# Optimization experiments

Hardware: AMD Instinct MI355X
Metric: run time of the kernel (lower is better)

Reference implementation:

```python
import jax, jax.numpy as jnp
from jax import lax
import numpy as np

N, E, L, H, B, R = 12800, 204800, 24, 128, 64, 8
VN, VA = 100, 20


def _p(key, *shape):
    return jax.random.normal(key, shape, dtype=jnp.float32) * 0.05


def setup_inputs() -> dict:
    key = jax.random.key(0)
    ks = jax.random.split(key, 32)
    inp = {
        'nodeTypes': jax.random.randint(ks[0], (N,), 0, VN),
        'edge_index': jax.random.randint(ks[1], (2, E), 0, N),
        'edge_attr': jax.random.randint(ks[2], (E,), 0, R),
        'bs': jnp.repeat(jnp.arange(B, dtype=jnp.int32), N // B),
        'sequence_input': jax.random.uniform(ks[3], (N, L), dtype=jnp.float32),
        'nodes_bs': jnp.full((B,), N // B, dtype=jnp.int32),
        'len_seq': jnp.full((B,), L, dtype=jnp.int32),
        'action_input': jax.random.randint(ks[4], (B,), 0, VA),
        # parameters (RGCN weights SHARED across the 2 layers, as in the source)
        'emb_nodes_w': _p(ks[5], VN, H),
        'emb_actions_w': _p(ks[6], VA, H),
        'rgcn_W': _p(ks[7], R, H, H),
        'rgcn_root': _p(ks[8], H, H),
        'rgcn_b': _p(ks[9], H),
        'gru_Wih': _p(ks[10], 3 * H, H),
        'gru_Whh': _p(ks[11], 3 * H, H),
        'gru_bih': _p(ks[12], 3 * H),
        'gru_bhh': _p(ks[13], 3 * H),
        'linA_w': _p(ks[14], H, H),
        'linA_b': _p(ks[15], H),
        'linAf_w': _p(ks[16], VA, H),
        'linAf_b': _p(ks[17], VA),
        'linN_w': _p(ks[18], H, 2 * H),
        'linN_b': _p(ks[19], H),
        'linNf_w': _p(ks[20], 1, H),
        'linNf_b': _p(ks[21], 1),
        'fin_w': _p(ks[22], H, H),
        'fin_b': _p(ks[23], H),
        'finf_w': _p(ks[24], 1, H),
        'finf_b': _p(ks[25], 1),
    }
    return inp


def _rgcn(x, src, dst, etype, W, Wroot, b):
    # PyG RGCNConv: per-relation mean aggregation, then per-relation weight, plus root + bias
    comb = dst * R + etype  # combined (node, relation) segment id
    msg = jax.ops.segment_sum(x[src], comb, num_segments=N * R)  # [N*R, H]
    cnt = jax.ops.segment_sum(jnp.ones((src.shape[0],), x.dtype), comb, num_segments=N * R)
    mean = (msg / jnp.maximum(cnt, 1.0)[:, None]).reshape(N, R, H)
    return jnp.einsum('nrh,rhd->nd', mean, W) + x @ Wroot + b


def _gru(x_seq, h0, Wih, Whh, bih, bhh):
    # torch GRU gate order: r, z, n ; x_seq [B, T, H]
    def step(h, x):
        gi = x @ Wih.T + bih
        gh = h @ Whh.T + bhh
        i_r, i_z, i_n = jnp.split(gi, 3, axis=-1)
        h_r, h_z, h_n = jnp.split(gh, 3, axis=-1)
        r = jax.nn.sigmoid(i_r + h_r)
        z = jax.nn.sigmoid(i_z + h_z)
        n = jnp.tanh(i_n + r * h_n)
        h_new = (1.0 - z) * n + z * h
        return h_new, h_new
    _, ys = lax.scan(step, h0, jnp.swapaxes(x_seq, 0, 1))
    return jnp.swapaxes(ys, 0, 1)


def _seg_softmax(x, seg, nseg):
    m = jax.ops.segment_max(x, seg, num_segments=nseg)
    e = jnp.exp(x - m[seg])
    s = jax.ops.segment_sum(e, seg, num_segments=nseg)
    return e / s[seg]


def reference(nodeTypes, edge_index, edge_attr, bs, sequence_input, nodes_bs, len_seq,
              action_input, emb_nodes_w, emb_actions_w, rgcn_W, rgcn_root, rgcn_b,
              gru_Wih, gru_Whh, gru_bih, gru_bhh, linA_w, linA_b, linAf_w, linAf_b,
              linN_w, linN_b, linNf_w, linNf_b, fin_w, fin_b, finf_w, finf_b):
    src, dst = edge_index[0], edge_index[1]
    x = emb_nodes_w[nodeTypes]
    for _ in range(2):  # shared-weight RGCN layers + ReLU
        x = jax.nn.relu(_rgcn(x, src, dst, edge_attr, rgcn_W, rgcn_root, rgcn_b))
    nodeEmb = x  # [N, H]

    cnt = jax.ops.segment_sum(jnp.ones((N,), x.dtype), bs, num_segments=B)
    h_G = jax.ops.segment_sum(nodeEmb, bs, num_segments=B) / cnt[:, None]  # [B, H]

    action = jax.nn.relu(h_G @ linA_w.T + linA_b) @ linAf_w.T + linAf_b  # [B, VA]
    final = jax.nn.sigmoid(jax.nn.relu(h_G @ fin_w.T + fin_b) @ finf_w.T + finf_b)  # [B, 1]

    sos = emb_actions_w[action_input][:, None, :]  # [B, 1, H]
    # scatter-sum of per-timestep weighted node embeddings -> [B, L, H]
    emb_seq = sequence_input[:, :, None] * nodeEmb[:, None, :]  # [N, L, H]
    agg = jax.ops.segment_sum(emb_seq, bs, num_segments=B)
    input_gru = jnp.concatenate([sos, agg], axis=1)[:, :L]  # len_seq == L drops last step
    seq = _gru(input_gru, h_G, gru_Wih, gru_Whh, gru_bih, gru_bhh)  # [B, L, H]

    # linNodes(cat(out_gru, nodeEmb)) computed without materializing the [N,L,2H] concat
    part1 = jnp.einsum('blh,oh->blo', seq, linN_w[:, :H])[bs]      # [N, L, H]
    part2 = nodeEmb @ linN_w[:, H:].T                               # [N, H]
    hidden = jax.nn.relu(part1 + part2[:, None, :] + linN_b)       # [N, L, H]
    logits = jnp.einsum('nlh,h->nl', hidden, linNf_w[0]) + linNf_b[0]  # [N, L]
    nodes_final = _seg_softmax(logits, bs, B)
    return (action, nodes_final, final)
```

## Files before the change

### kernel.cpp

```cpp
#include <hip/hip_runtime.h>
#include <math.h>

#define NN 12800
#define NE 204800
#define LL 24
#define HH 128
#define BB 64
#define RR 8
#define VAx 20
#define KC 1152
#define CHK 8
#define PS 16

typedef __attribute__((ext_vector_type(8))) short bf16x8;
typedef __attribute__((ext_vector_type(4))) float f32x4;

__device__ inline unsigned short f2bf(float f) {
  unsigned u = __float_as_uint(f);
  unsigned r = u + 0x7FFF + ((u >> 16) & 1);
  return (unsigned short)(r >> 16);
}
__device__ inline float bf2f(unsigned short s) {
  return __uint_as_float(((unsigned)s) << 16);
}
__device__ inline unsigned packbf(float lo, float hi) {
  return (unsigned)f2bf(lo) | ((unsigned)f2bf(hi) << 16);
}

__global__ void k_prep(const float* __restrict__ rgcnW, const float* __restrict__ rgcnRoot,
                       unsigned short* __restrict__ wcatT,
                       const float* __restrict__ linN_w, unsigned short* __restrict__ linN2bt,
                       const float* __restrict__ Wih, unsigned short* __restrict__ Wihbt,
                       const float* __restrict__ Whh, float* __restrict__ WhhT,
                       const float* __restrict__ linA_w, float* __restrict__ linAT,
                       const float* __restrict__ fin_w, float* __restrict__ finT,
                       unsigned short* __restrict__ linN1bt,
                       const int* __restrict__ nt, const float* __restrict__ embN,
                       unsigned int* __restrict__ x, int* __restrict__ deg) {
  int idx = blockIdx.x * 256 + threadIdx.x;
  if (idx < HH * KC) {
    int d = idx / KC, k = idx - d * KC;
    float v = (k < 1024) ? rgcnW[(k >> 7) * (HH * HH) + (k & 127) * HH + d]
                         : rgcnRoot[(k - 1024) * HH + d];
    wcatT[idx] = f2bf(v);
    return;
  }
  idx -= HH * KC;
  if (idx < HH * HH) {
    int d = idx >> 7, k = idx & 127;
    linN2bt[idx] = f2bf(linN_w[d * 2 * HH + HH + k]);
    return;
  }
  idx -= HH * HH;
  if (idx < 3 * HH * HH) {
    Wihbt[idx] = f2bf(Wih[idx]);
    return;
  }
  idx -= 3 * HH * HH;
  if (idx < 3 * HH * HH) {
    int r = idx / HH, c = idx - r * HH;
    WhhT[c * 384 + r] = Whh[r * HH + c];
    return;
  }
  idx -= 3 * HH * HH;
  if (idx < HH * HH) {
    int r = idx >> 7, c = idx & 127;
    linAT[c * HH + r] = linA_w[r * HH + c];
    return;
  }
  idx -= HH * HH;
  if (idx < HH * HH) {
    int r = idx >> 7, c = idx & 127;
    finT[c * HH + r] = fin_w[r * HH + c];
    return;
  }
  idx -= HH * HH;
  if (idx < HH * HH) {
    int o = idx >> 7, k = idx & 127;
    linN1bt[idx] = f2bf(linN_w[o * 2 * HH + k]);
    return;
  }
  idx -= HH * HH;
  if (idx < NN * 64) {
    int n = idx >> 6, p = idx & 63;
    const float* e = embN + (size_t)nt[n] * HH + p * 2;
    x[idx] = packbf(e[0], e[1]);
    return;
  }
  idx -= NN * 64;
  if (idx < NN * PS) deg[idx] = 0;
}
#define PREP_TOTAL (HH * KC + HH * HH + 3 * HH * HH + 3 * HH * HH + HH * HH + HH * HH + HH * HH + NN * 64 + NN * PS)

__global__ void k_count(const int* __restrict__ edst, int* __restrict__ deg,
                        const int* __restrict__ bs, int* __restrict__ bptr) {
  int i = blockIdx.x * 256 + threadIdx.x;
  if (i < NE) atomicAdd(&deg[edst[i] * PS], 1);
  if (i < NN) {
    int b = bs[i];
    if (i == 0 || bs[i - 1] != b) bptr[b] = i;
    if (i == NN - 1) bptr[BB] = NN;
  }
}

__global__ __launch_bounds__(1024) void k_scane(const int* __restrict__ deg,
                                                int* __restrict__ indptr,
                                                int* __restrict__ cur) {
  __shared__ int ws[16];
  int tid = threadIdx.x;
  const int per = (NN + 1023) >> 10;
  int i0 = tid * per;
  int s = 0;
  for (int k = 0; k < per; ++k) {
    int i = i0 + k;
    if (i < NN) s += deg[i * PS];
  }
  int lane = tid & 63, wv = tid >> 6;
  int incl = s;
#pragma unroll
  for (int off = 1; off < 64; off <<= 1) {
    int t = __shfl_up(incl, off);
    if (lane >= off) incl += t;
  }
  if (lane == 63) ws[wv] = incl;
  __syncthreads();
  if (tid < 16) {
    int v = ws[tid];
    int inc = v;
#pragma unroll
    for (int off = 1; off < 16; off <<= 1) {
      int t = __shfl_up(inc, off);
      if (tid >= off) inc += t;
    }
    ws[tid] = inc - v;
  }
  __syncthreads();
  int run = ws[wv] + incl - s;
  for (int k = 0; k < per; ++k) {
    int i = i0 + k;
    if (i < NN) {
      indptr[i] = run;
      cur[i * PS] = run;
      run += deg[i * PS];
      if (i == NN - 1) indptr[NN] = run;
    }
  }
}

__global__ void k_scattere(const int* __restrict__ esrc, const int* __restrict__ edst,
                           const int* __restrict__ erel, int* __restrict__ cur,
                           int* __restrict__ esort) {
  int i = blockIdx.x * 256 + threadIdx.x;
  if (i >= NE) return;
  int p = atomicAdd(&cur[edst[i] * PS], 1);
  esort[p] = esrc[i] | (erel[i] << 16);
}

__global__ __launch_bounds__(256) void k_agg(const unsigned int* __restrict__ x,
                                             const int* __restrict__ indptr,
                                             const int* __restrict__ esort,
                                             unsigned int* __restrict__ A, int n0, int nc) {
  int wid = ((blockIdx.x * 256) + threadIdx.x) >> 6;
  int lane = threadIdx.x & 63;
  if (wid >= nc) return;
  int n = n0 + wid;
  float a0=0,a1=0,a2=0,a3=0,a4=0,a5=0,a6=0,a7=0;
  float b0=0,b1=0,b2=0,b3=0,b4=0,b5=0,b6=0,b7=0;
  int c0=0,c1=0,c2=0,c3=0,c4=0,c5=0,c6=0,c7=0;
  int e0 = indptr[n], e1 = indptr[n + 1];

#define ACCV(RV, VV)                                                              \
  {                                                                               \
    float v0_ = bf2f((unsigned short)((VV) & 0xFFFF));                            \
    float v1_ = bf2f((unsigned short)((VV) >> 16));                               \
    switch (RV) {                                                                 \
      case 0: a0 += v0_; b0 += v1_; c0++; break;                                  \
      case 1: a1 += v0_; b1 += v1_; c1++; break;                                  \
      case 2: a2 += v0_; b2 += v1_; c2++; break;                                  \
      case 3: a3 += v0_; b3 += v1_; c3++; break;                                  \
      case 4: a4 += v0_; b4 += v1_; c4++; break;                                  \
      case 5: a5 += v0_; b5 += v1_; c5++; break;                                  \
      case 6: a6 += v0_; b6 += v1_; c6++; break;                                  \
      default: a7 += v0_; b7 += v1_; c7++; break;                                 \
    }                                                                             \
  }

  int e = e0;
  for (; e + 8 <= e1; e += 8) {
    int pk0 = esort[e + 0], pk1 = esort[e + 1], pk2 = esort[e + 2], pk3 = esort[e + 3];
    int pk4 = esort[e + 4], pk5 = esort[e + 5], pk6 = esort[e + 6], pk7 = esort[e + 7];
    unsigned v0 = x[(size_t)(pk0 & 0xFFFF) * 64 + lane];
    unsigned v1 = x[(size_t)(pk1 & 0xFFFF) * 64 + lane];
    unsigned v2 = x[(size_t)(pk2 & 0xFFFF) * 64 + lane];
    unsigned v3 = x[(size_t)(pk3 & 0xFFFF) * 64 + lane];
    unsigned v4 = x[(size_t)(pk4 & 0xFFFF) * 64 + lane];
    unsigned v5 = x[(size_t)(pk5 & 0xFFFF) * 64 + lane];
    unsigned v6 = x[(size_t)(pk6 & 0xFFFF) * 64 + lane];
    unsigned v7 = x[(size_t)(pk7 & 0xFFFF) * 64 + lane];
    ACCV(pk0 >> 16, v0);
    ACCV(pk1 >> 16, v1);
    ACCV(pk2 >> 16, v2);
    ACCV(pk3 >> 16, v3);
    ACCV(pk4 >> 16, v4);
    ACCV(pk5 >> 16, v5);
    ACCV(pk6 >> 16, v6);
    ACCV(pk7 >> 16, v7);
  }
  for (; e + 4 <= e1; e += 4) {
    int pk0 = esort[e + 0], pk1 = esort[e + 1], pk2 = esort[e + 2], pk3 = esort[e + 3];
    unsigned v0 = x[(size_t)(pk0 & 0xFFFF) * 64 + lane];
    unsigned v1 = x[(size_t)(pk1 & 0xFFFF) * 64 + lane];
    unsigned v2 = x[(size_t)(pk2 & 0xFFFF) * 64 + lane];
    unsigned v3 = x[(size_t)(pk3 & 0xFFFF) * 64 + lane];
    ACCV(pk0 >> 16, v0);
    ACCV(pk1 >> 16, v1);
    ACCV(pk2 >> 16, v2);
    ACCV(pk3 >> 16, v3);
  }
  for (; e < e1; ++e) {
    int pk = esort[e];
    unsigned v = x[(size_t)(pk & 0xFFFF) * 64 + lane];
    ACCV(pk >> 16, v);
  }
#undef ACCV

  unsigned int* Ar = A + (size_t)wid * (KC / 2);
  float i0 = 1.0f / (float)(c0 > 0 ? c0 : 1);
  float i1 = 1.0f / (float)(c1 > 0 ? c1 : 1);
  float i2 = 1.0f / (float)(c2 > 0 ? c2 : 1);
  float i3 = 1.0f / (float)(c3 > 0 ? c3 : 1);
  float i4 = 1.0f / (float)(c4 > 0 ? c4 : 1);
  float i5 = 1.0f / (float)(c5 > 0 ? c5 : 1);
  float i6 = 1.0f / (float)(c6 > 0 ? c6 : 1);
  float i7 = 1.0f / (float)(c7 > 0 ? c7 : 1);
  Ar[0 * 64 + lane] = packbf(a0 * i0, b0 * i0);
  Ar[1 * 64 + lane] = packbf(a1 * i1, b1 * i1);
  Ar[2 * 64 + lane] = packbf(a2 * i2, b2 * i2);
  Ar[3 * 64 + lane] = packbf(a3 * i3, b3 * i3);
  Ar[4 * 64 + lane] = packbf(a4 * i4, b4 * i4);
  Ar[5 * 64 + lane] = packbf(a5 * i5, b5 * i5);
  Ar[6 * 64 + lane] = packbf(a6 * i6, b6 * i6);
  Ar[7 * 64 + lane] = packbf(a7 * i7, b7 * i7);
  Ar[512 + lane] = x[n * 64 + lane];
}

__global__ __launch_bounds__(256) void k_mgemm_rg32(const unsigned short* __restrict__ Abf,
                                                    const unsigned short* __restrict__ BTbf,
                                                    const float* __restrict__ bias,
                                                    unsigned short* __restrict__ C) {
  __shared__ unsigned int ldsu[(4096 + 16384) / 4];
  char* ldsc = (char*)ldsu;
  int tid = threadIdx.x;
  int m0 = blockIdx.x * 32;
  int w = tid >> 6, l = tid & 63;
  int lrow = l & 15, lg = l >> 4;
  int rowg = w & 1, colg = w >> 1;
  f32x4 acc[4] = {};

  const char* Ab = (const char*)Abf;
  const char* Bb = (const char*)BTbf;
  for (int kt = 0; kt < KC / 64; ++kt) {
    int k0 = kt << 6;
    {
      int slot = tid;
      int row = slot >> 3;
      int colb = (slot & 7) << 4;
      size_t srcb = ((size_t)(m0 + row) * KC + k0) * 2 + (size_t)(colb ^ ((row & 7) << 4));
      __builtin_amdgcn_global_load_lds((const unsigned int*)(Ab + srcb),
                                       (unsigned int*)(ldsc + slot * 16), 16, 0, 0);
    }
#pragma unroll
    for (int i = 0; i < 4; ++i) {
      int slot = i * 256 + tid;
      int row = slot >> 3;
      int colb = (slot & 7) << 4;
      size_t srcb = ((size_t)row * KC + k0) * 2 + (size_t)(colb ^ ((row & 7) << 4));
      __builtin_amdgcn_global_load_lds((const unsigned int*)(Bb + srcb),
                                       (unsigned int*)(ldsc + 4096 + slot * 16), 16, 0, 0);
    }
    __syncthreads();
#pragma unroll
    for (int h = 0; h < 2; ++h) {
      int arow = rowg * 16 + lrow;
      bf16x8 af = *(const bf16x8*)(ldsc + arow * 128 +
                                   ((h * 64 + lg * 16) ^ ((arow & 7) << 4)));
#pragma unroll
      for (int c = 0; c < 4; ++c) {
        int brow = (colg * 4 + c) * 16 + lrow;
        bf16x8 bfr = *(const bf16x8*)(ldsc + 4096 + brow * 128 +
                                      ((h * 64 + lg * 16) ^ ((brow & 7) << 4)));
        acc[c] = __builtin_amdgcn_mfma_f32_16x16x32_bf16(af, bfr, acc[c], 0, 0, 0);
      }
    }
    __syncthreads();
  }
#pragma unroll
  for (int c = 0; c < 4; ++c) {
    int gn = (colg * 4 + c) * 16 + lrow;
    float bv = bias[gn];
#pragma unroll
    for (int r = 0; r < 4; ++r) {
      int gm = m0 + rowg * 16 + lg * 4 + r;
      float v = fmaxf(acc[c][r] + bv, 0.f);
      C[(size_t)gm * HH + gn] = f2bf(v);
    }
  }
}

template <int OUTMODE>
__global__ __launch_bounds__(256) void k_mgemm(const unsigned short* __restrict__ Abf, int lda,
                                               const unsigned short* __restrict__ BTbf, int ldb,
                                               const float* __restrict__ bias,
                                               void* __restrict__ C, int ldc, int M, int K) {
  __shared__ unsigned int ldsu[(8192 + 16384) / 4];
  char* ldsc = (char*)ldsu;
  int tid = threadIdx.x;
  int m0 = blockIdx.x * 64;
  int n0c = blockIdx.y * 128;
  int w = tid >> 6, l = tid & 63;
  int lrow = l & 15, lg = l >> 4;
  f32x4 acc[8] = {};

  const char* Ab = (const char*)Abf;
  const char* Bb = (const char*)(BTbf + (size_t)n0c * ldb);
  int KT = K >> 6;
  for (int kt = 0; kt < KT; ++kt) {
    int k0 = kt << 6;
#pragma unroll
    for (int i = 0; i < 2; ++i) {
      int slot = i * 256 + tid;
      int row = slot >> 3;
      int colb = (slot & 7) << 4;
      int gr = m0 + row;
      gr = gr < M ? gr : M - 1;
      size_t srcb = ((size_t)gr * lda + k0) * 2 + (size_t)(colb ^ ((row & 7) << 4));
      __builtin_amdgcn_global_load_lds((const unsigned int*)(Ab + srcb),
                                       (unsigned int*)(ldsc + slot * 16), 16, 0, 0);
    }
#pragma unroll
    for (int i = 0; i < 4; ++i) {
      int slot = i * 256 + tid;
      int row = slot >> 3;
      int colb = (slot & 7) << 4;
      size_t srcb = ((size_t)row * ldb + k0) * 2 + (size_t)(colb ^ ((row & 7) << 4));
      __builtin_amdgcn_global_load_lds((const unsigned int*)(Bb + srcb),
                                       (unsigned int*)(ldsc + 8192 + slot * 16), 16, 0, 0);
    }
    __syncthreads();
#pragma unroll
    for (int h = 0; h < 2; ++h) {
      int arow = w * 16 + lrow;
      bf16x8 af = *(const bf16x8*)(ldsc + arow * 128 +
                                   ((h * 64 + lg * 16) ^ ((arow & 7) << 4)));
#pragma unroll
      for (int c = 0; c < 8; ++c) {
        int brow = c * 16 + lrow;
        bf16x8 bf = *(const bf16x8*)(ldsc + 8192 + brow * 128 +
                                     ((h * 64 + lg * 16) ^ ((brow & 7) << 4)));
        acc[c] = __builtin_amdgcn_mfma_f32_16x16x32_bf16(af, bf, acc[c], 0, 0, 0);
      }
    }
    __syncthreads();
  }
#pragma unroll
  for (int c = 0; c < 8; ++c) {
#pragma unroll
    for (int r = 0; r < 4; ++r) {
      int gm = m0 + w * 16 + lg * 4 + r;
      if (gm >= M) continue;
      int gn = n0c + c * 16 + lrow;
      float v = acc[c][r];
      if (OUTMODE == 1) {
        v = fmaxf(v + bias[gn], 0.f);
        ((unsigned short*)C)[(size_t)gm * ldc + gn] = f2bf(v);
      } else if (OUTMODE == 2) {
        ((float*)C)[(size_t)gm * ldc + gn] = v + bias[gn];
      } else {
        ((float*)C)[(size_t)gm * ldc + gn] = v;
      }
    }
  }
}

__global__ __launch_bounds__(256) void k_mgemm_gp(const unsigned short* __restrict__ ig,
                                                  const unsigned short* __restrict__ Wihbt,
                                                  const float* __restrict__ bih,
                                                  float* __restrict__ gi,
                                                  const unsigned short* __restrict__ nodeEmb,
                                                  const unsigned short* __restrict__ linN2bt,
                                                  float* __restrict__ part2) {
  __shared__ unsigned int ldsu[(8192 + 16384) / 4];
  char* ldsc = (char*)ldsu;
  int tid = threadIdx.x;
  int bid = blockIdx.x;
  const unsigned short* Abf;
  const unsigned short* BTbf;
  const float* bias;
  float* Cf;
  int m0, ldc, withbias;
  const int GIB = (BB * LL / 64) * 3;
  if (bid < GIB) {
    int mb = bid / 3, nc = bid % 3;
    Abf = ig;
    BTbf = Wihbt + (size_t)(nc * 128) * HH;
    bias = bih + nc * 128;
    Cf = gi + nc * 128;
    m0 = mb * 64;
    ldc = 3 * HH;
    withbias = 1;
  } else {
    Abf = nodeEmb;
    BTbf = linN2bt;
    bias = nullptr;
    Cf = part2;
    m0 = (bid - GIB) * 64;
    ldc = HH;
    withbias = 0;
  }
  int w = tid >> 6, l = tid & 63;
  int lrow = l & 15, lg = l >> 4;
  f32x4 acc[8] = {};
  const char* Ab = (const char*)Abf;
  const char* Bb = (const char*)BTbf;
  for (int kt = 0; kt < 2; ++kt) {
    int k0 = kt << 6;
#pragma unroll
    for (int i = 0; i < 2; ++i) {
      int slot = i * 256 + tid;
      int row = slot >> 3;
      int colb = (slot & 7) << 4;
      size_t srcb = ((size_t)(m0 + row) * HH + k0) * 2 + (size_t)(colb ^ ((row & 7) << 4));
      __builtin_amdgcn_global_load_lds((const unsigned int*)(Ab + srcb),
                                       (unsigned int*)(ldsc + slot * 16), 16, 0, 0);
    }
#pragma unroll
    for (int i = 0; i < 4; ++i) {
      int slot = i * 256 + tid;
      int row = slot >> 3;
      int colb = (slot & 7) << 4;
      size_t srcb = ((size_t)row * HH + k0) * 2 + (size_t)(colb ^ ((row & 7) << 4));
      __builtin_amdgcn_global_load_lds((const unsigned int*)(Bb + srcb),
                                       (unsigned int*)(ldsc + 8192 + slot * 16), 16, 0, 0);
    }
    __syncthreads();
#pragma unroll
    for (int h = 0; h < 2; ++h) {
      int arow = w * 16 + lrow;
      bf16x8 af = *(const bf16x8*)(ldsc + arow * 128 +
                                   ((h * 64 + lg * 16) ^ ((arow & 7) << 4)));
#pragma unroll
      for (int c = 0; c < 8; ++c) {
        int brow = c * 16 + lrow;
        bf16x8 bfr = *(const bf16x8*)(ldsc + 8192 + brow * 128 +
                                      ((h * 64 + lg * 16) ^ ((brow & 7) << 4)));
        acc[c] = __builtin_amdgcn_mfma_f32_16x16x32_bf16(af, bfr, acc[c], 0, 0, 0);
      }
    }
    __syncthreads();
  }
#pragma unroll
  for (int c = 0; c < 8; ++c) {
    int gn = c * 16 + lrow;
    float bv = withbias ? bias[gn] : 0.f;
#pragma unroll
    for (int r = 0; r < 4; ++r) {
      int gm = m0 + w * 16 + lg * 4 + r;
      Cf[(size_t)gm * ldc + gn] = acc[c][r] + bv;
    }
  }
}

__global__ __launch_bounds__(256) void k_aggS_part(const float* __restrict__ seqin,
                                                   const unsigned short* __restrict__ x,
                                                   const int* __restrict__ bptr,
                                                   float* __restrict__ part) {
  int bc = blockIdx.x, b = bc >> 3, c = bc & 7;
  int h = threadIdx.x & 127, l0 = threadIdx.x >> 7;
  int i0 = bptr[b], i1 = bptr[b + 1];
  int len = i1 - i0;
  int per = (len + CHK - 1) / CHK;
  int j0 = i0 + c * per;
  int j1 = j0 + per;
  if (j1 > i1) j1 = i1;
  float acc[12] = {};
  float esum = 0.f;
  for (int n = j0; n < j1; ++n) {
    float e = bf2f(x[n * HH + h]);
    esum += e;
    const float* srow = seqin + (size_t)n * LL;
#pragma unroll
    for (int t = 0; t < 12; ++t) acc[t] = fmaf(srow[l0 + 2 * t], e, acc[t]);
  }
  float* p = part + (size_t)bc * 25 * HH + h;
#pragma unroll
  for (int t = 0; t < 12; ++t) p[(l0 + 2 * t) * HH] = acc[t];
  if (l0 == 0) p[24 * HH] = esum;
}

__global__ void k_aggS_red(const float* __restrict__ part, const int* __restrict__ bptr,
                           const float* __restrict__ embA, const int* __restrict__ act,
                           unsigned short* __restrict__ ig, float* __restrict__ hG) {
  int idx = blockIdx.x * 256 + threadIdx.x;
  if (idx >= BB * 25 * HH) return;
  int h = idx & 127;
  int rem = idx >> 7;
  int l = rem % 25, b = rem / 25;
  if (l == 23) {
    ig[((size_t)b * LL) * HH + h] = f2bf(embA[(size_t)act[b] * HH + h]);
    return;
  }
  float s = 0.f;
#pragma unroll
  for (int c = 0; c < CHK; ++c) s += part[(((size_t)(b * CHK + c)) * 25 + l) * HH + h];
  if (l == 24) {
    int len = bptr[b + 1] - bptr[b];
    hG[b * HH + h] = s / (float)len;
  } else {
    ig[((size_t)b * LL + l + 1) * HH + h] = f2bf(s);
  }
}

__global__ __launch_bounds__(128) void k_heads(const float* __restrict__ hG,
                                               const float* __restrict__ linAT,
                                               const float* __restrict__ linA_b,
                                               const float* __restrict__ linAf_w,
                                               const float* __restrict__ linAf_b,
                                               const float* __restrict__ finT,
                                               const float* __restrict__ fin_b,
                                               const float* __restrict__ finf_w,
                                               const float* __restrict__ finf_b,
                                               float* __restrict__ outA,
                                               float* __restrict__ outF) {
  int b = blockIdx.x >> 1, which = blockIdx.x & 1, j = threadIdx.x;
  __shared__ float hsh[HH], t1[HH];
  hsh[j] = hG[b * HH + j];
  __syncthreads();
  const float* Wt = which ? finT : linAT;
  const float* bb = which ? fin_b : linA_b;
  float s = bb[j];
  for (int k = 0; k < HH; ++k) s = fmaf(hsh[k], Wt[k * HH + j], s);
  t1[j] = fmaxf(s, 0.f);
  __syncthreads();
  if (which == 0) {
    if (j < VAx) {
      float o = linAf_b[j];
      for (int k = 0; k < HH; ++k) o = fmaf(t1[k], linAf_w[j * HH + k], o);
      outA[b * VAx + j] = o;
    }
  } else if (j == 0) {
    float o = finf_b[0];
    for (int k = 0; k < HH; ++k) o = fmaf(t1[k], finf_w[k], o);
    outF[b] = 1.f / (1.f + expf(-o));
  }
}

__global__ __launch_bounds__(384) void k_gru(const float* __restrict__ gi,
                                             const float* __restrict__ WhhT,
                                             const float* __restrict__ bhh,
                                             const float* __restrict__ hG,
                                             unsigned short* __restrict__ seqout) {
  int b = blockIdx.x, tid = threadIdx.x;
  int gate = tid >> 7, j = tid & 127;
  __shared__ float h[HH];
  __shared__ float sz[HH], sg[HH];
  float w[HH];
#pragma unroll
  for (int k = 0; k < HH; ++k) w[k] = WhhT[k * 384 + tid];
  float bh = bhh[tid];
  if (tid < HH) h[tid] = hG[b * HH + tid];
  __syncthreads();
  const float* gib = gi + (size_t)b * LL * 384;
  for (int t = 0; t < LL; ++t) {
    float giv = gib[t * 384 + tid];
    float gin = (gate == 0) ? gib[t * 384 + 256 + j] : 0.f;
    float hj = h[j];
    float g0 = 0.f, g1 = 0.f, g2 = 0.f, g3 = 0.f;
    const float4* h4 = (const float4*)h;
#pragma unroll
    for (int k4 = 0; k4 < HH / 4; ++k4) {
      float4 hv = h4[k4];
      g0 = fmaf(w[4 * k4 + 0], hv.x, g0);
      g1 = fmaf(w[4 * k4 + 1], hv.y, g1);
      g2 = fmaf(w[4 * k4 + 2], hv.z, g2);
      g3 = fmaf(w[4 * k4 + 3], hv.w, g3);
    }
    float g = bh + ((g0 + g1) + (g2 + g3));
    float r = 0.f;
    if (gate == 0) {
      r = 1.f / (1.f + expf(-(giv + g)));
    } else if (gate == 1) {
      sz[j] = 1.f / (1.f + expf(-(giv + g)));
    } else {
      sg[j] = g;
    }
    __syncthreads();
    if (gate == 0) {
      float n = tanhf(gin + r * sg[j]);
      float z = sz[j];
      float hn = (1.f - z) * n + z * hj;
      h[j] = hn;
      seqout[((size_t)b * LL + t) * HH + j] = f2bf(hn);
    }
    __syncthreads();
  }
}

__global__ __launch_bounds__(256) void k_logits(const float* __restrict__ part1,
                                                const float* __restrict__ part2,
                                                const float* __restrict__ linN_b,
                                                const float* __restrict__ linNf_w,
                                                const float* __restrict__ linNf_b,
                                                const int* __restrict__ bs,
                                                float* __restrict__ logits) {
  int wid = ((blockIdx.x * 256) + threadIdx.x) >> 6;
  int lane = threadIdx.x & 63;
  if (wid >= NN) return;
  int n = wid;
  int b = bs[n];
  float p2a = part2[n * HH + lane] + linN_b[lane];
  float p2b = part2[n * HH + 64 + lane] + linN_b[64 + lane];
  float wa = linNf_w[lane], wb = linNf_w[64 + lane];
  const float* p1 = part1 + (size_t)b * LL * HH;
  float bf = linNf_b[0];
  for (int l = 0; l < LL; ++l) {
    float v = fmaxf(p1[l * HH + lane] + p2a, 0.f) * wa +
              fmaxf(p1[l * HH + 64 + lane] + p2b, 0.f) * wb;
#pragma unroll
    for (int off = 32; off > 0; off >>= 1) v += __shfl_down(v, off);
    if (lane == 0) logits[n * LL + l] = v + bf;
  }
}

__global__ __launch_bounds__(64) void k_softmax(const float* __restrict__ logits,
                                                const int* __restrict__ bptr,
                                                float* __restrict__ outN) {
  int b = blockIdx.x / LL, l = blockIdx.x % LL;
  int lane = threadIdx.x;
  int i0 = bptr[b], i1 = bptr[b + 1];
  float m = -1e30f;
  for (int i = i0 + lane; i < i1; i += 64) m = fmaxf(m, logits[i * LL + l]);
#pragma unroll
  for (int off = 32; off > 0; off >>= 1) m = fmaxf(m, __shfl_xor(m, off));
  float s = 0.f;
  for (int i = i0 + lane; i < i1; i += 64) s += expf(logits[i * LL + l] - m);
#pragma unroll
  for (int off = 32; off > 0; off >>= 1) s += __shfl_xor(s, off);
  float inv = 1.f / s;
  for (int i = i0 + lane; i < i1; i += 64) {
    outN[i * LL + l] = expf(logits[i * LL + l] - m) * inv;
  }
}

extern "C" void kernel_launch(void* const* d_in, const int* in_sizes, int n_in,
                              void* d_out, int out_size, void* d_ws, size_t ws_size,
                              hipStream_t stream) {
  const int* nodeTypes = (const int*)d_in[0];
  const int* esrc = (const int*)d_in[1];
  const int* edst = esrc + NE;
  const int* erel = (const int*)d_in[2];
  const int* bs = (const int*)d_in[3];
  const float* seqin = (const float*)d_in[4];
  const int* actin = (const int*)d_in[7];
  const float* embN = (const float*)d_in[8];
  const float* embA = (const float*)d_in[9];
  const float* rgcnW = (const float*)d_in[10];
  const float* rgcnRoot = (const float*)d_in[11];
  const float* rgcnB = (const float*)d_in[12];
  const float* Wih = (const float*)d_in[13];
  const float* Whh = (const float*)d_in[14];
  const float* bih = (const float*)d_in[15];
  const float* bhh = (const float*)d_in[16];
  const float* linA_w = (const float*)d_in[17];
  const float* linA_b = (const float*)d_in[18];
  const float* linAf_w = (const float*)d_in[19];
  const float* linAf_b = (const float*)d_in[20];
  const float* linN_w = (const float*)d_in[21];
  const float* linN_b = (const float*)d_in[22];
  const float* linNf_w = (const float*)d_in[23];
  const float* linNf_b = (const float*)d_in[24];
  const float* fin_w = (const float*)d_in[25];
  const float* fin_b = (const float*)d_in[26];
  const float* finf_w = (const float*)d_in[27];
  const float* finf_b = (const float*)d_in[28];

  float* outA = (float*)d_out;
  float* outNodes = outA + BB * VAx;
  float* outF = outNodes + (size_t)NN * LL;

  char* basep = (char*)d_ws;
  size_t off = 0;
  auto alloc = [&](size_t bytes) -> void* {
    void* p = basep + off;
    off = (off + bytes + 255) & ~(size_t)255;
    return p;
  };

  unsigned int* x = (unsigned int*)alloc(sizeof(unsigned int) * NN * 64);
  unsigned int* x2 = (unsigned int*)alloc(sizeof(unsigned int) * NN * 64);
  float* hG = (float*)alloc(sizeof(float) * BB * HH);
  unsigned short* wcatT = (unsigned short*)alloc(sizeof(unsigned short) * HH * KC);
  unsigned short* linN2bt = (unsigned short*)alloc(sizeof(unsigned short) * HH * HH);
  unsigned short* Wihbt = (unsigned short*)alloc(sizeof(unsigned short) * 3 * HH * HH);
  unsigned short* linN1bt = (unsigned short*)alloc(sizeof(unsigned short) * HH * HH);
  float* WhhT = (float*)alloc(sizeof(float) * HH * 3 * HH);
  float* linAT = (float*)alloc(sizeof(float) * HH * HH);
  float* finT = (float*)alloc(sizeof(float) * HH * HH);
  float* part = (float*)alloc(sizeof(float) * BB * CHK * 25 * HH);
  unsigned short* ig = (unsigned short*)alloc(sizeof(unsigned short) * BB * LL * HH);
  float* gi = (float*)alloc(sizeof(float) * BB * LL * 3 * HH);
  unsigned short* seqb = (unsigned short*)alloc(sizeof(unsigned short) * BB * LL * HH);
  float* part1 = (float*)alloc(sizeof(float) * BB * LL * HH);
  float* part2 = (float*)alloc(sizeof(float) * NN * HH);
  float* logitsB = (float*)alloc(sizeof(float) * NN * LL);
  int* deg = (int*)alloc(sizeof(int) * NN * PS);
  int* cur = (int*)alloc(sizeof(int) * NN * PS);
  int* indptr = (int*)alloc(sizeof(int) * (NN + 1));
  int* esort = (int*)alloc(sizeof(int) * NE);
  int* bptr = (int*)alloc(sizeof(int) * (BB + 1));

  size_t remain = (ws_size > off) ? (ws_size - off) : 0;
  int NCk = NN;
  while ((size_t)NCk * KC * 2 > remain && NCk > 100) NCk >>= 1;
  unsigned int* A = (unsigned int*)alloc((size_t)NCk * (KC / 2) * sizeof(unsigned int));

  k_prep<<<(PREP_TOTAL + 255) / 256, 256, 0, stream>>>(
      rgcnW, rgcnRoot, wcatT, linN_w, linN2bt, Wih, Wihbt, Whh, WhhT, linA_w, linAT,
      fin_w, finT, linN1bt, nodeTypes, embN, x, deg);

  k_count<<<(NE + 255) / 256, 256, 0, stream>>>(edst, deg, bs, bptr);
  k_scane<<<1, 1024, 0, stream>>>(deg, indptr, cur);
  k_scattere<<<(NE + 255) / 256, 256, 0, stream>>>(esrc, edst, erel, cur, esort);

  const unsigned int* xin = x;
  unsigned int* xout = x2;
  for (int layer = 0; layer < 2; ++layer) {
    for (int n0 = 0; n0 < NN; n0 += NCk) {
      int nc = NN - n0 < NCk ? NN - n0 : NCk;
      k_agg<<<(nc + 3) / 4, 256, 0, stream>>>(xin, indptr, esort, A, n0, nc);
      k_mgemm_rg32<<<nc / 32, 256, 0, stream>>>(
          (const unsigned short*)A, wcatT, rgcnB,
          (unsigned short*)xout + (size_t)n0 * HH);
    }
    const unsigned int* t = xin;
    xin = xout;
    xout = (unsigned int*)t;
  }
  const unsigned short* nodeEmb = (const unsigned short*)xin;

  k_aggS_part<<<BB * CHK, 256, 0, stream>>>(seqin, nodeEmb, bptr, part);
  k_aggS_red<<<(BB * 25 * HH + 255) / 256, 256, 0, stream>>>(part, bptr, embA, actin, ig, hG);

  k_mgemm_gp<<<(BB * LL / 64) * 3 + NN / 64, 256, 0, stream>>>(ig, Wihbt, bih, gi,
                                                               nodeEmb, linN2bt, part2);

  k_heads<<<2 * BB, HH, 0, stream>>>(hG, linAT, linA_b, linAf_w, linAf_b, finT, fin_b,
                                     finf_w, finf_b, outA, outF);

  k_gru<<<BB, 384, 0, stream>>>(gi, WhhT, bhh, hG, seqb);

  {
    dim3 g((BB * LL) / 64, 1);
    k_mgemm<0><<<g, 256, 0, stream>>>(seqb, HH, linN1bt, HH, nullptr, (void*)part1, HH,
                                      BB * LL, HH);
  }
  k_logits<<<NN / 4, 256, 0, stream>>>(part1, part2, linN_b, linNf_w, linNf_b, bs, logitsB);
  k_softmax<<<BB * LL, 64, 0, stream>>>(logitsB, bptr, outNodes);
}
```

Measured before the change: 248.5 us.

## Fuse edge counting into prep, heads into GEMM, logits with softmax

Folds the degree counting and batch pointer computation into the prep kernel, using a memset to zero degrees. The small MLP heads run as extra blocks of the GEMM kernel. The logits and segment softmax become a single per-(graph,timestep) kernel that keeps logits in shared memory, removing the intermediate logits buffer and several launches. The fused softmax kernel re-reads part2 for every timestep and assumes at most 256 nodes per graph.

```diff
diff --git a/kernel.cpp b/kernel.cpp
--- a/kernel.cpp
+++ b/kernel.cpp
@@ -36,7 +36,9 @@
                        const float* __restrict__ fin_w, float* __restrict__ finT,
                        unsigned short* __restrict__ linN1bt,
                        const int* __restrict__ nt, const float* __restrict__ embN,
-                       unsigned int* __restrict__ x, int* __restrict__ deg) {
+                       unsigned int* __restrict__ x, int* __restrict__ deg,
+                       const int* __restrict__ edst, const int* __restrict__ bs,
+                       int* __restrict__ bptr) {
   int idx = blockIdx.x * 256 + threadIdx.x;
   if (idx < HH * KC) {
     int d = idx / KC, k = idx - d * KC;
@@ -88,20 +90,18 @@
     return;
   }
   idx -= NN * 64;
-  if (idx < NN * PS) deg[idx] = 0;
-}
-#define PREP_TOTAL (HH * KC + HH * HH + 3 * HH * HH + 3 * HH * HH + HH * HH + HH * HH + HH * HH + NN * 64 + NN * PS)
-
-__global__ void k_count(const int* __restrict__ edst, int* __restrict__ deg,
-                        const int* __restrict__ bs, int* __restrict__ bptr) {
-  int i = blockIdx.x * 256 + threadIdx.x;
-  if (i < NE) atomicAdd(&deg[edst[i] * PS], 1);
-  if (i < NN) {
-    int b = bs[i];
-    if (i == 0 || bs[i - 1] != b) bptr[b] = i;
-    if (i == NN - 1) bptr[BB] = NN;
-  }
-}
+  if (idx < NE) {
+    atomicAdd(&deg[edst[idx] * PS], 1);
+    return;
+  }
+  idx -= NE;
+  if (idx < NN) {
+    int b = bs[idx];
+    if (idx == 0 || bs[idx - 1] != b) bptr[b] = idx;
+    if (idx == NN - 1) bptr[BB] = NN;
+  }
+}
+#define PREP_TOTAL (HH * KC + HH * HH + 3 * HH * HH + 3 * HH * HH + HH * HH + HH * HH + HH * HH + NN * 64 + NE + NN)
 
 __global__ __launch_bounds__(1024) void k_scane(const int* __restrict__ deg,
                                                 int* __restrict__ indptr,
@@ -382,23 +382,62 @@
   }
 }
 
-__global__ __launch_bounds__(256) void k_mgemm_gp(const unsigned short* __restrict__ ig,
+__global__ __launch_bounds__(256) void k_gp_heads(const unsigned short* __restrict__ ig,
                                                   const unsigned short* __restrict__ Wihbt,
                                                   const float* __restrict__ bih,
                                                   float* __restrict__ gi,
                                                   const unsigned short* __restrict__ nodeEmb,
                                                   const unsigned short* __restrict__ linN2bt,
-                                                  float* __restrict__ part2) {
+                                                  float* __restrict__ part2,
+                                                  const float* __restrict__ hG,
+                                                  const float* __restrict__ linAT,
+                                                  const float* __restrict__ linA_b,
+                                                  const float* __restrict__ linAf_w,
+                                                  const float* __restrict__ linAf_b,
+                                                  const float* __restrict__ finT,
+                                                  const float* __restrict__ fin_b,
+                                                  const float* __restrict__ finf_w,
+                                                  const float* __restrict__ finf_b,
+                                                  float* __restrict__ outA,
+                                                  float* __restrict__ outF) {
+  int tid = threadIdx.x;
+  int bid = blockIdx.x;
+  const int GIB = (BB * LL / 64) * 3;
+  const int GEMMB = GIB + NN / 64;
+  if (bid >= GEMMB) {
+    int hb = bid - GEMMB;
+    int b = hb >> 1, which = hb & 1, j = tid;
+    __shared__ float hsh[HH], t1[HH];
+    if (j < HH) hsh[j] = hG[b * HH + j];
+    __syncthreads();
+    if (j < HH) {
+      const float* Wt = which ? finT : linAT;
+      const float* bb = which ? fin_b : linA_b;
+      float s = bb[j];
+      for (int k = 0; k < HH; ++k) s = fmaf(hsh[k], Wt[k * HH + j], s);
+      t1[j] = fmaxf(s, 0.f);
+    }
+    __syncthreads();
+    if (which == 0) {
+      if (j < VAx) {
+        float o = linAf_b[j];
+        for (int k = 0; k < HH; ++k) o = fmaf(t1[k], linAf_w[j * HH + k], o);
+        outA[b * VAx + j] = o;
+      }
+    } else if (j == 0) {
+      float o = finf_b[0];
+      for (int k = 0; k < HH; ++k) o = fmaf(t1[k], finf_w[k], o);
+      outF[b] = 1.f / (1.f + expf(-o));
+    }
+    return;
+  }
   __shared__ unsigned int ldsu[(8192 + 16384) / 4];
   char* ldsc = (char*)ldsu;
-  int tid = threadIdx.x;
-  int bid = blockIdx.x;
   const unsigned short* Abf;
   const unsigned short* BTbf;
   const float* bias;
   float* Cf;
   int m0, ldc, withbias;
-  const int GIB = (BB * LL / 64) * 3;
   if (bid < GIB) {
     int mb = bid / 3, nc = bid % 3;
     Abf = ig;
@@ -520,40 +559,6 @@
   }
 }
 
-__global__ __launch_bounds__(128) void k_heads(const float* __restrict__ hG,
-                                               const float* __restrict__ linAT,
-                                               const float* __restrict__ linA_b,
-                                               const float* __restrict__ linAf_w,
-                                               const float* __restrict__ linAf_b,
-                                               const float* __restrict__ finT,
-                                               const float* __restrict__ fin_b,
-                                               const float* __restrict__ finf_w,
-                                               const float* __restrict__ finf_b,
-                                               float* __restrict__ outA,
-                                               float* __restrict__ outF) {
-  int b = blockIdx.x >> 1, which = blockIdx.x & 1, j = threadIdx.x;
-  __shared__ float hsh[HH], t1[HH];
-  hsh[j] = hG[b * HH + j];
-  __syncthreads();
-  const float* Wt = which ? finT : linAT;
-  const float* bb = which ? fin_b : linA_b;
-  float s = bb[j];
-  for (int k = 0; k < HH; ++k) s = fmaf(hsh[k], Wt[k * HH + j], s);
-  t1[j] = fmaxf(s, 0.f);
-  __syncthreads();
-  if (which == 0) {
-    if (j < VAx) {
-      float o = linAf_b[j];
-      for (int k = 0; k < HH; ++k) o = fmaf(t1[k], linAf_w[j * HH + k], o);
-      outA[b * VAx + j] = o;
-    }
-  } else if (j == 0) {
-    float o = finf_b[0];
-    for (int k = 0; k < HH; ++k) o = fmaf(t1[k], finf_w[k], o);
-    outF[b] = 1.f / (1.f + expf(-o));
-  }
-}
-
 __global__ __launch_bounds__(384) void k_gru(const float* __restrict__ gi,
                                              const float* __restrict__ WhhT,
                                              const float* __restrict__ bhh,
@@ -605,50 +610,49 @@
   }
 }
 
-__global__ __launch_bounds__(256) void k_logits(const float* __restrict__ part1,
-                                                const float* __restrict__ part2,
-                                                const float* __restrict__ linN_b,
-                                                const float* __restrict__ linNf_w,
-                                                const float* __restrict__ linNf_b,
-                                                const int* __restrict__ bs,
-                                                float* __restrict__ logits) {
-  int wid = ((blockIdx.x * 256) + threadIdx.x) >> 6;
-  int lane = threadIdx.x & 63;
-  if (wid >= NN) return;
-  int n = wid;
-  int b = bs[n];
-  float p2a = part2[n * HH + lane] + linN_b[lane];
-  float p2b = part2[n * HH + 64 + lane] + linN_b[64 + lane];
-  float wa = linNf_w[lane], wb = linNf_w[64 + lane];
-  const float* p1 = part1 + (size_t)b * LL * HH;
+__global__ __launch_bounds__(256) void k_logsm(const float* __restrict__ part1,
+                                               const float* __restrict__ part2,
+                                               const float* __restrict__ linN_b,
+                                               const float* __restrict__ linNf_w,
+                                               const float* __restrict__ linNf_b,
+                                               const int* __restrict__ bptr,
+                                               float* __restrict__ outN) {
+  int bl = blockIdx.x;
+  int b = bl / LL, l = bl % LL;
+  __shared__ float p1b[HH], wsh[HH], lg[256], red[8];
+  int tid = threadIdx.x;
+  int w = tid >> 6, lane = tid & 63;
+  if (tid < HH) {
+    p1b[tid] = part1[((size_t)b * LL + l) * HH + tid] + linN_b[tid];
+    wsh[tid] = linNf_w[tid];
+  }
+  __syncthreads();
+  int i0 = bptr[b], i1 = bptr[b + 1];
+  int len = i1 - i0;
   float bf = linNf_b[0];
-  for (int l = 0; l < LL; ++l) {
-    float v = fmaxf(p1[l * HH + lane] + p2a, 0.f) * wa +
-              fmaxf(p1[l * HH + 64 + lane] + p2b, 0.f) * wb;
+  for (int i = i0 + w; i < i1; i += 4) {
+    const float* p2 = part2 + (size_t)i * HH;
+    float v = fmaxf(p1b[lane] + p2[lane], 0.f) * wsh[lane] +
+              fmaxf(p1b[64 + lane] + p2[64 + lane], 0.f) * wsh[64 + lane];
 #pragma unroll
     for (int off = 32; off > 0; off >>= 1) v += __shfl_down(v, off);
-    if (lane == 0) logits[n * LL + l] = v + bf;
-  }
-}
-
-__global__ __launch_bounds__(64) void k_softmax(const float* __restrict__ logits,
-                                                const int* __restrict__ bptr,
-                                                float* __restrict__ outN) {
-  int b = blockIdx.x / LL, l = blockIdx.x % LL;
-  int lane = threadIdx.x;
-  int i0 = bptr[b], i1 = bptr[b + 1];
-  float m = -1e30f;
-  for (int i = i0 + lane; i < i1; i += 64) m = fmaxf(m, logits[i * LL + l]);
+    if (lane == 0) lg[i - i0] = v + bf;
+  }
+  __syncthreads();
+  float m = (tid < len) ? lg[tid] : -1e30f;
 #pragma unroll
   for (int off = 32; off > 0; off >>= 1) m = fmaxf(m, __shfl_xor(m, off));
-  float s = 0.f;
-  for (int i = i0 + lane; i < i1; i += 64) s += expf(logits[i * LL + l] - m);
+  if (lane == 0) red[w] = m;
+  __syncthreads();
+  m = fmaxf(fmaxf(red[0], red[1]), fmaxf(red[2], red[3]));
+  float e = (tid < len) ? expf(lg[tid] - m) : 0.f;
+  float s = e;
 #pragma unroll
   for (int off = 32; off > 0; off >>= 1) s += __shfl_xor(s, off);
-  float inv = 1.f / s;
-  for (int i = i0 + lane; i < i1; i += 64) {
-    outN[i * LL + l] = expf(logits[i * LL + l] - m) * inv;
-  }
+  if (lane == 0) red[4 + w] = s;
+  __syncthreads();
+  s = (red[4] + red[5]) + (red[6] + red[7]);
+  if (tid < len) outN[(size_t)(i0 + tid) * LL + l] = e / s;
 }
 
 extern "C" void kernel_launch(void* const* d_in, const int* in_sizes, int n_in,
@@ -711,7 +715,6 @@
   unsigned short* seqb = (unsigned short*)alloc(sizeof(unsigned short) * BB * LL * HH);
   float* part1 = (float*)alloc(sizeof(float) * BB * LL * HH);
   float* part2 = (float*)alloc(sizeof(float) * NN * HH);
-  float* logitsB = (float*)alloc(sizeof(float) * NN * LL);
   int* deg = (int*)alloc(sizeof(int) * NN * PS);
   int* cur = (int*)alloc(sizeof(int) * NN * PS);
   int* indptr = (int*)alloc(sizeof(int) * (NN + 1));
@@ -723,11 +726,11 @@
   while ((size_t)NCk * KC * 2 > remain && NCk > 100) NCk >>= 1;
   unsigned int* A = (unsigned int*)alloc((size_t)NCk * (KC / 2) * sizeof(unsigned int));
 
+  hipMemsetAsync(deg, 0, sizeof(int) * NN * PS, stream);
   k_prep<<<(PREP_TOTAL + 255) / 256, 256, 0, stream>>>(
       rgcnW, rgcnRoot, wcatT, linN_w, linN2bt, Wih, Wihbt, Whh, WhhT, linA_w, linAT,
-      fin_w, finT, linN1bt, nodeTypes, embN, x, deg);
-
-  k_count<<<(NE + 255) / 256, 256, 0, stream>>>(edst, deg, bs, bptr);
+      fin_w, finT, linN1bt, nodeTypes, embN, x, deg, edst, bs, bptr);
+
   k_scane<<<1, 1024, 0, stream>>>(deg, indptr, cur);
   k_scattere<<<(NE + 255) / 256, 256, 0, stream>>>(esrc, edst, erel, cur, esort);
 
@@ -750,11 +753,9 @@
   k_aggS_part<<<BB * CHK, 256, 0, stream>>>(seqin, nodeEmb, bptr, part);
   k_aggS_red<<<(BB * 25 * HH + 255) / 256, 256, 0, stream>>>(part, bptr, embA, actin, ig, hG);
 
-  k_mgemm_gp<<<(BB * LL / 64) * 3 + NN / 64, 256, 0, stream>>>(ig, Wihbt, bih, gi,
-                                                               nodeEmb, linN2bt, part2);
-
-  k_heads<<<2 * BB, HH, 0, stream>>>(hG, linAT, linA_b, linAf_w, linAf_b, finT, fin_b,
-                                     finf_w, finf_b, outA, outF);
+  k_gp_heads<<<(BB * LL / 64) * 3 + NN / 64 + 2 * BB, 256, 0, stream>>>(
+      ig, Wihbt, bih, gi, nodeEmb, linN2bt, part2, hG, linAT, linA_b, linAf_w, linAf_b,
+      finT, fin_b, finf_w, finf_b, outA, outF);
 
   k_gru<<<BB, 384, 0, stream>>>(gi, WhhT, bhh, hG, seqb);
 
@@ -763,6 +764,6 @@
     k_mgemm<0><<<g, 256, 0, stream>>>(seqb, HH, linN1bt, HH, nullptr, (void*)part1, HH,
                                       BB * LL, HH);
   }
-  k_logits<<<NN / 4, 256, 0, stream>>>(part1, part2, linN_b, linNf_w, linNf_b, bs, logitsB);
-  k_softmax<<<BB * LL, 64, 0, stream>>>(logitsB, bptr, outNodes);
-}
+  k_logsm<<<BB * LL, 256, 0, stream>>>(part1, part2, linN_b, linNf_w, linNf_b, bptr,
+                                       outNodes);
+}
```

Measured after the change: 243.5 us (median of 2 runs). 2.0% less time.
